# Kernel tuning notes

Measured on AMD Instinct MI355X. Metric: run time of the kernel, lower is better.

The kernel has to match this reference:

```python
import jax, jax.numpy as jnp
import numpy as np

N = 10000       # nodes
F_IN = 512      # input_features
E_DIM = 256     # embedding_features
H0, H1 = 512, 256  # fc layer widths (layers=[512,256]); fc input = 2*E_DIM = 512
N_EDGES = 160000


def setup_inputs() -> dict:
    key = jax.random.key(0)
    ks = jax.random.split(key, 10)
    feature = jax.random.normal(ks[0], (N, F_IN), jnp.float32)
    edge_src = jax.random.randint(ks[1], (N_EDGES,), 0, N, jnp.int32)
    edge_dst = jax.random.randint(ks[2], (N_EDGES,), 0, N, jnp.int32)
    def lin(k, fan_in, fan_out):
        return jax.random.normal(k, (fan_in, fan_out), jnp.float32) / np.sqrt(fan_in).astype(np.float32)
    We = lin(ks[3], F_IN, E_DIM);     be = jnp.zeros((E_DIM,), jnp.float32)
    W0 = lin(ks[4], 2 * E_DIM, H0);   b0 = jnp.zeros((H0,), jnp.float32)
    W1 = lin(ks[5], H0, H1);          b1 = jnp.zeros((H1,), jnp.float32)
    Wlk = lin(ks[6], H1, 1);          blk = jnp.zeros((1,), jnp.float32)
    Wa = lin(ks[7], H1, 2);           ba = jnp.zeros((2,), jnp.float32)
    return dict(feature=feature, We=We, be=be, W0=W0, b0=b0, W1=W1, b1=b1,
                Wlk=Wlk, blk=blk, Wa=Wa, ba=ba,
                edge_src=edge_src, edge_dst=edge_dst)


def reference(feature, We, be, W0, b0, W1, b1, Wlk, blk, Wa, ba, edge_src, edge_dst):
    # get_embedding: Linear + relu
    emb = jax.nn.relu(feature @ We + be)                      # [N, E]
    # Each node i has its neighbor entries plus one 'ending' entry paired with zeros
    seg = jnp.concatenate([edge_src, jnp.arange(N, dtype=edge_src.dtype)])     # [T]
    dst_all = jnp.concatenate([edge_dst, jnp.full((N,), -1, edge_dst.dtype)])  # -1 = ending sentinel
    nbr = jnp.concatenate([emb[edge_dst], jnp.zeros((N, E_DIM), emb.dtype)], axis=0)
    s = jnp.concatenate([emb[seg], nbr], axis=-1)             # [T, 2E]
    # fc MLP, then lk head
    h = jax.nn.relu(jax.nn.relu(s @ W0 + b0) @ W1 + b1)       # [T, H1]
    lk = (h @ Wlk + blk)[:, 0]                                # [T]
    # Deterministic greedy pick per node (argmax of lk == argmax of softmax(lk))
    best = jax.ops.segment_max(lk, seg, num_segments=N)       # [N]
    T = lk.shape[0]
    cand = jnp.where(lk == best[seg], jnp.arange(T, dtype=jnp.int32), -1)
    win = jax.ops.segment_max(cand, seg, num_segments=N)      # winning entry index per node
    chosen = dst_all[win]                                     # chosen neighbor (-1 = ending)
    # action head on the winning pair feature; argmax(softmax(logits)) == argmax(logits)
    logits = h[win] @ Wa + ba                                 # [N, 2]
    at = jnp.argmax(logits, axis=-1)
    do_upd = (chosen >= 0) & (at == 1)
    safe = jnp.clip(chosen, 0, N - 1)
    # hv = mean(feature_origin[i], feature_origin[chosen]) then re-embed
    mean_feat = 0.5 * (feature + feature[safe])               # [N, F]
    new_val = jax.nn.relu(mean_feat @ We + be)                # [N, E]
    tgt = jnp.where(do_upd, safe, N)                          # N = out of range -> dropped
    return emb.at[tgt].set(new_val, mode='drop')
```

## Files before the change

### kernel.cpp

```cpp
#include <hip/hip_runtime.h>
#include <stdint.h>

#define N_NODES 10000
#define F_IN    512
#define E_DIM   256
#define H0D     512
#define H1D     256
#define N_EDGES 160000
#define T_TOT   (N_EDGES + N_NODES)

#define MARGIN_LK 4e-3f
#define MARGIN_L  4e-3f
#define LIST_CAP 60000
#define FIX_GRID 512
#define LP 40

typedef _Float16 f16;
typedef __attribute__((ext_vector_type(8))) _Float16 f16x8;
typedef __attribute__((ext_vector_type(4))) _Float16 f16x4;
typedef __attribute__((ext_vector_type(4))) float f32x4;

__device__ __forceinline__ unsigned int f2ord(float f) {
    unsigned int u = __float_as_uint(f);
    return (u & 0x80000000u) ? ~u : (u | 0x80000000u);
}
__device__ __forceinline__ float ord2f(unsigned int o) {
    unsigned int u = (o & 0x80000000u) ? (o & 0x7fffffffu) : ~o;
    return __uint_as_float(u);
}

__device__ __forceinline__ int seg_of(int t, const int* esrc) {
    return (t < N_EDGES) ? esrc[t] : t - N_EDGES;
}

__global__ void k_prep_all(const float* __restrict__ We,
                           const float* __restrict__ W1,
                           const float* __restrict__ W0,
                           f16* __restrict__ WeC_h, f16* __restrict__ WeC_l,
                           f16* __restrict__ W1C_h, f16* __restrict__ W1C_l,
                           f16* __restrict__ W0C_h, f16* __restrict__ W0C_l) {
    int b = blockIdx.x;
    int n = threadIdx.x;
    const float* W;
    int ld, rowoff, colbase, c;
    f16 *dh_base, *dl_base;
    if (b < 16) {
        W = We; ld = E_DIM; rowoff = 0; colbase = 0; c = b;
        dh_base = WeC_h; dl_base = WeC_l;
    } else if (b < 32) {
        W = W1; ld = H1D; rowoff = 0; colbase = 0; c = b - 16;
        dh_base = W1C_h; dl_base = W1C_l;
    } else {
        int g = (b - 32) >> 3; c = (b - 32) & 7;
        rowoff = (g >= 2) ? 256 : 0; colbase = (g & 1) * 256;
        W = W0; ld = H0D;
        dh_base = W0C_h + (size_t)g * 8 * 256 * 32;
        dl_base = W0C_l + (size_t)g * 8 * 256 * 32;
    }
    f16* dh = dh_base + ((size_t)c * 256 + n) * 32;
    f16* dl = dl_base + ((size_t)c * 256 + n) * 32;
    const float* src = W + (size_t)(rowoff + c * 32) * ld + colbase + n;
#pragma unroll
    for (int kk = 0; kk < 32; kk++) {
        float w = src[(size_t)kk * ld];
        f16 h = (f16)w;
        f16 l = (f16)(w - (float)h);
        dh[kk] = h;
        dl[kk] = l;
    }
}

__global__ __launch_bounds__(256, 2) void k1_split(
        const float* __restrict__ feat, const f16* __restrict__ Bh_g,
        const f16* __restrict__ Bl_g, const float* __restrict__ be,
        float* __restrict__ Z, float* __restrict__ out) {
    __shared__ f16 Ah[32 * LP], Al_[32 * LP];
    const int tid = threadIdx.x;
    const int wave = tid >> 6, lane = tid & 63;
    const int quad = lane >> 4, l15 = lane & 15;
    const int mbase = blockIdx.x * 32;
    const int arow = tid >> 3, apos = tid & 7;
    const int gm_a = mbase + arow;
    const float* Arow = feat + (size_t)gm_a * F_IN + apos * 4;
    const bool rowok = (gm_a < N_NODES);

    f32x4 acc[2][4];
#pragma unroll
    for (int i = 0; i < 2; i++)
#pragma unroll
        for (int j = 0; j < 4; j++) acc[i][j] = (f32x4){0.f, 0.f, 0.f, 0.f};

    f16x8 bh[4], bl[4], bhn[4], bln[4];
#pragma unroll
    for (int ct = 0; ct < 4; ct++) {
        size_t o = ((size_t)(wave * 64 + ct * 16 + l15)) * 32 + quad * 8;
        bh[ct] = *(const f16x8*)(Bh_g + o);
        bl[ct] = *(const f16x8*)(Bl_g + o);
    }
    float4 a = rowok ? *(const float4*)(Arow) : make_float4(0.f, 0.f, 0.f, 0.f);

    for (int c = 0; c < 16; c++) {
        f16x4 hv, lv;
        float av[4] = {a.x, a.y, a.z, a.w};
#pragma unroll
        for (int q = 0; q < 4; q++) {
            f16 h = (f16)av[q];
            hv[q] = h;
            lv[q] = (f16)(av[q] - (float)h);
        }
        *(f16x4*)(Ah + arow * LP + apos * 4) = hv;
        *(f16x4*)(Al_ + arow * LP + apos * 4) = lv;
        if (c + 1 < 16) {
            a = rowok ? *(const float4*)(Arow + (c + 1) * 32)
                      : make_float4(0.f, 0.f, 0.f, 0.f);
#pragma unroll
            for (int ct = 0; ct < 4; ct++) {
                size_t o = ((size_t)((c + 1) * 256 + wave * 64 + ct * 16 + l15)) * 32 + quad * 8;
                bhn[ct] = *(const f16x8*)(Bh_g + o);
                bln[ct] = *(const f16x8*)(Bl_g + o);
            }
        }
        __syncthreads();
        f16x8 afh[2], afl[2];
#pragma unroll
        for (int rt = 0; rt < 2; rt++) {
            afh[rt] = *(const f16x8*)(Ah + (rt * 16 + l15) * LP + quad * 8);
            afl[rt] = *(const f16x8*)(Al_ + (rt * 16 + l15) * LP + quad * 8);
        }
#pragma unroll
        for (int rt = 0; rt < 2; rt++)
#pragma unroll
            for (int ct = 0; ct < 4; ct++) {
                acc[rt][ct] = __builtin_amdgcn_mfma_f32_16x16x32_f16(
                    afh[rt], bh[ct], acc[rt][ct], 0, 0, 0);
                acc[rt][ct] = __builtin_amdgcn_mfma_f32_16x16x32_f16(
                    afl[rt], bh[ct], acc[rt][ct], 0, 0, 0);
                acc[rt][ct] = __builtin_amdgcn_mfma_f32_16x16x32_f16(
                    afh[rt], bl[ct], acc[rt][ct], 0, 0, 0);
            }
        __syncthreads();
#pragma unroll
        for (int ct = 0; ct < 4; ct++) { bh[ct] = bhn[ct]; bl[ct] = bln[ct]; }
    }

#pragma unroll
    for (int ct = 0; ct < 4; ct++) {
        int n = wave * 64 + ct * 16 + l15;
        float bb = be[n];
#pragma unroll
        for (int rt = 0; rt < 2; rt++)
#pragma unroll
            for (int reg = 0; reg < 4; reg++) {
                int gm = mbase + rt * 16 + quad * 4 + reg;
                if (gm < N_NODES) {
                    float z = acc[rt][ct][reg] + bb;
                    Z[(size_t)gm * E_DIM + n] = z;
                    out[(size_t)gm * E_DIM + n] = fmaxf(z, 0.f);
                }
            }
    }
}

__global__ __launch_bounds__(256, 3) void k2_split(
        const float* __restrict__ emb, const f16* __restrict__ W0Ch,
        const f16* __restrict__ W0Cl, const float* __restrict__ b0,
        f16* __restrict__ Ph, f16* __restrict__ Pl,
        f16* __restrict__ Qh, f16* __restrict__ Ql) {
    __shared__ f16 Ah[64 * LP], Al_[64 * LP];
    const int tid = threadIdx.x;
    const int wave = tid >> 6, lane = tid & 63;
    const int quad = lane >> 4, l15 = lane & 15;
    const int mbase = blockIdx.x * 64;
    const int g = blockIdx.y;
    const int isQ = (g >= 2);
    const int colbase = (g & 1) * 256;
    const int arow = tid >> 2, akp = tid & 3;
    const int gm_a = mbase + arow;
    const float* Arow = emb + (size_t)gm_a * E_DIM + akp * 8;
    const bool rowok = (gm_a < N_NODES);
    const f16* Bh_g = W0Ch + (size_t)g * 8 * 256 * 32;
    const f16* Bl_g = W0Cl + (size_t)g * 8 * 256 * 32;

    f32x4 acc[4][4];
#pragma unroll
    for (int i = 0; i < 4; i++)
#pragma unroll
        for (int j = 0; j < 4; j++) acc[i][j] = (f32x4){0.f, 0.f, 0.f, 0.f};

    f16x8 bh[4], bl[4], bhn[4], bln[4];
#pragma unroll
    for (int ct = 0; ct < 4; ct++) {
        size_t o = ((size_t)(wave * 64 + ct * 16 + l15)) * 32 + quad * 8;
        bh[ct] = *(const f16x8*)(Bh_g + o);
        bl[ct] = *(const f16x8*)(Bl_g + o);
    }
    float4 a0 = make_float4(0.f, 0.f, 0.f, 0.f), a1 = a0;
    if (rowok) { a0 = *(const float4*)(Arow); a1 = *(const float4*)(Arow + 4); }

    for (int c = 0; c < 8; c++) {
        f16x8 hv, lv;
        float av[8] = {a0.x, a0.y, a0.z, a0.w, a1.x, a1.y, a1.z, a1.w};
#pragma unroll
        for (int q = 0; q < 8; q++) {
            f16 h = (f16)av[q];
            hv[q] = h;
            lv[q] = (f16)(av[q] - (float)h);
        }
        *(f16x8*)(Ah + arow * LP + akp * 8) = hv;
        *(f16x8*)(Al_ + arow * LP + akp * 8) = lv;
        if (c + 1 < 8) {
            if (rowok) {
                a0 = *(const float4*)(Arow + (c + 1) * 32);
                a1 = *(const float4*)(Arow + (c + 1) * 32 + 4);
            }
#pragma unroll
            for (int ct = 0; ct < 4; ct++) {
                size_t o = ((size_t)((c + 1) * 256 + wave * 64 + ct * 16 + l15)) * 32 + quad * 8;
                bhn[ct] = *(const f16x8*)(Bh_g + o);
                bln[ct] = *(const f16x8*)(Bl_g + o);
            }
        }
        __syncthreads();
        f16x8 afh[4], afl[4];
#pragma unroll
        for (int rt = 0; rt < 4; rt++) {
            afh[rt] = *(const f16x8*)(Ah + (rt * 16 + l15) * LP + quad * 8);
            afl[rt] = *(const f16x8*)(Al_ + (rt * 16 + l15) * LP + quad * 8);
        }
#pragma unroll
        for (int rt = 0; rt < 4; rt++)
#pragma unroll
            for (int ct = 0; ct < 4; ct++) {
                acc[rt][ct] = __builtin_amdgcn_mfma_f32_16x16x32_f16(
                    afh[rt], bh[ct], acc[rt][ct], 0, 0, 0);
                acc[rt][ct] = __builtin_amdgcn_mfma_f32_16x16x32_f16(
                    afl[rt], bh[ct], acc[rt][ct], 0, 0, 0);
                acc[rt][ct] = __builtin_amdgcn_mfma_f32_16x16x32_f16(
                    afh[rt], bl[ct], acc[rt][ct], 0, 0, 0);
            }
        __syncthreads();
#pragma unroll
        for (int ct = 0; ct < 4; ct++) { bh[ct] = bhn[ct]; bl[ct] = bln[ct]; }
    }

    f16* dh = isQ ? Qh : Ph;
    f16* dl = isQ ? Ql : Pl;
#pragma unroll
    for (int ct = 0; ct < 4; ct++) {
        int n = wave * 64 + ct * 16 + l15;
        float bb = isQ ? 0.f : b0[colbase + n];
#pragma unroll
        for (int rt = 0; rt < 4; rt++)
#pragma unroll
            for (int reg = 0; reg < 4; reg++) {
                int gm = mbase + rt * 16 + quad * 4 + reg;
                if (gm < N_NODES) {
                    float v = acc[rt][ct][reg] + bb;
                    f16 h = (f16)v;
                    dh[(size_t)gm * H0D + colbase + n] = h;
                    dl[(size_t)gm * H0D + colbase + n] = (f16)(v - (float)h);
                }
            }
    }
}

__global__ __launch_bounds__(256, 3) void k3_f16(
        const f16* __restrict__ Pf, const f16* __restrict__ Qf,
        const f16* __restrict__ W1Bh, const float* __restrict__ b1,
        const float* __restrict__ Wlk, const float* __restrict__ blkp,
        const float* __restrict__ Wa, const float* __restrict__ ba,
        const int* __restrict__ esrc, const int* __restrict__ edst,
        unsigned long long* __restrict__ keys, float* __restrict__ lk_app,
        float* __restrict__ logits) {
    __shared__ f16 Ah[64 * LP];
    __shared__ float redA[64][5], redB[64][5], redC[64][5];
    __shared__ int s_seg[64], s_dst[64];
    const int tid = threadIdx.x;
    const int wave = tid >> 6, lane = tid & 63;
    const int quad = lane >> 4, l15 = lane & 15;
    const int tbase = blockIdx.x * 64;

    if (tid < 64) {
        int t = tbase + tid;
        int s = 0, d = -1;
        if (t < N_EDGES) { s = esrc[t]; d = edst[t]; }
        else if (t < T_TOT) { s = t - N_EDGES; }
        s_seg[tid] = s;
        s_dst[tid] = d;
    }
    __syncthreads();

    const int arow = tid >> 2, akp = tid & 3;
    const int sA = s_seg[arow], dA = s_dst[arow];
    const f16* Prow = Pf + (size_t)sA * H0D + akp * 8;
    const f16* Qrow = Qf + (size_t)(dA >= 0 ? dA : 0) * H0D + akp * 8;
    const bool hasQ = (dA >= 0);
    const f16x8 zero8 = (f16x8)(f16)0;

    f32x4 acc[4][4];
#pragma unroll
    for (int i = 0; i < 4; i++)
#pragma unroll
        for (int j = 0; j < 4; j++) acc[i][j] = (f32x4){0.f, 0.f, 0.f, 0.f};

    f16x8 pa0 = *(const f16x8*)(Prow);
    f16x8 qa0 = hasQ ? *(const f16x8*)(Qrow) : zero8;
    f16x8 pa1 = *(const f16x8*)(Prow + 32);
    f16x8 qa1 = hasQ ? *(const f16x8*)(Qrow + 32) : zero8;
    f16x8 bf[4], bfn[4];
#pragma unroll
    for (int ct = 0; ct < 4; ct++)
        bf[ct] = *(const f16x8*)(W1Bh + ((size_t)(wave * 64 + ct * 16 + l15)) * 32 + quad * 8);

    for (int c = 0; c < 16; c++) {
        f16x8 hv;
#pragma unroll
        for (int q = 0; q < 8; q++) {
            f16 s = pa0[q] + qa0[q];
            hv[q] = (s > (f16)0) ? s : (f16)0;
        }
        *(f16x8*)(Ah + arow * LP + akp * 8) = hv;
        pa0 = pa1; qa0 = qa1;
        if (c + 2 < 16) {
            pa1 = *(const f16x8*)(Prow + (c + 2) * 32);
            qa1 = hasQ ? *(const f16x8*)(Qrow + (c + 2) * 32) : zero8;
        }
        if (c + 1 < 16) {
#pragma unroll
            for (int ct = 0; ct < 4; ct++)
                bfn[ct] = *(const f16x8*)(W1Bh +
                    ((size_t)((c + 1) * 256 + wave * 64 + ct * 16 + l15)) * 32 + quad * 8);
        }
        __syncthreads();
        f16x8 af[4];
#pragma unroll
        for (int rt = 0; rt < 4; rt++)
            af[rt] = *(const f16x8*)(Ah + (rt * 16 + l15) * LP + quad * 8);
#pragma unroll
        for (int rt = 0; rt < 4; rt++)
#pragma unroll
            for (int ct = 0; ct < 4; ct++)
                acc[rt][ct] = __builtin_amdgcn_mfma_f32_16x16x32_f16(
                    af[rt], bf[ct], acc[rt][ct], 0, 0, 0);
        __syncthreads();
#pragma unroll
        for (int ct = 0; ct < 4; ct++) bf[ct] = bfn[ct];
    }

    float wl[4], wa0[4], wa1[4], bb[4];
#pragma unroll
    for (int ct = 0; ct < 4; ct++) {
        int n = wave * 64 + ct * 16 + l15;
        wl[ct] = Wlk[n];
        wa0[ct] = Wa[2 * n];
        wa1[ct] = Wa[2 * n + 1];
        bb[ct] = b1[n];
    }
#pragma unroll
    for (int rt = 0; rt < 4; rt++) {
#pragma unroll
        for (int reg = 0; reg < 4; reg++) {
            float plk = 0.f, p0 = 0.f, p1 = 0.f;
#pragma unroll
            for (int ct = 0; ct < 4; ct++) {
                float h = fmaxf(acc[rt][ct][reg] + bb[ct], 0.f);
                plk = fmaf(h, wl[ct], plk);
                p0 = fmaf(h, wa0[ct], p0);
                p1 = fmaf(h, wa1[ct], p1);
            }
#pragma unroll
            for (int off = 8; off >= 1; off >>= 1) {
                plk += __shfl_xor(plk, off);
                p0 += __shfl_xor(p0, off);
                p1 += __shfl_xor(p1, off);
            }
            if (l15 == 0) {
                int row = rt * 16 + quad * 4 + reg;
                redA[row][wave] = plk;
                redB[row][wave] = p0;
                redC[row][wave] = p1;
            }
        }
    }
    __syncthreads();
    if (tid < 64) {
        int t = tbase + tid;
        if (t < T_TOT) {
            float lk = redA[tid][0] + redA[tid][1] + redA[tid][2] + redA[tid][3] + blkp[0];
            float l0 = redB[tid][0] + redB[tid][1] + redB[tid][2] + redB[tid][3] + ba[0];
            float l1 = redC[tid][0] + redC[tid][1] + redC[tid][2] + redC[tid][3] + ba[1];
            lk_app[t] = lk;
            logits[2 * t] = l0;
            logits[2 * t + 1] = l1;
            unsigned long long key =
                ((unsigned long long)f2ord(lk) << 32) | (unsigned int)t;
            atomicMax(keys + s_seg[tid], key);
        }
    }
}

__global__ void k_gb(const float* __restrict__ lk_app,
                     const unsigned long long* __restrict__ keys,
                     const int* __restrict__ esrc,
                     const float* __restrict__ logits,
                     int* __restrict__ seg_flag,
                     int* __restrict__ list, int* __restrict__ count) {
    int t = blockIdx.x * 256 + threadIdx.x;
    if (t < T_TOT) {
        int seg = seg_of(t, esrc);
        unsigned long long k = keys[seg];
        int tw = (int)(k & 0xFFFFFFFFull);
        if (t != tw) {
            float best = ord2f((unsigned int)(k >> 32));
            if (lk_app[t] >= best - MARGIN_LK) {
                int idx = atomicAdd(count, 1);
                if (idx < LIST_CAP) list[idx] = t;
                if (atomicExch(seg_flag + seg, 1) == 0) {
                    int idx2 = atomicAdd(count, 1);
                    if (idx2 < LIST_CAP) list[idx2] = tw;
                }
            }
        }
    }
    if (t < N_NODES) {
        int tw = (int)(keys[t] & 0xFFFFFFFFull);
        float g = fabsf(logits[2 * tw + 1] - logits[2 * tw]);
        if (g < MARGIN_L) {
            int idx = atomicAdd(count, 1);
            if (idx < LIST_CAP) list[idx] = tw;
        }
    }
}

__global__ __launch_bounds__(256, 2) void k_fix2(
        const f16* __restrict__ Ph, const f16* __restrict__ Pl,
        const f16* __restrict__ Qh, const f16* __restrict__ Ql,
        const f16* __restrict__ W1Ch, const f16* __restrict__ W1Cl,
        const float* __restrict__ b1, const float* __restrict__ Wlk,
        const float* __restrict__ blkp, const float* __restrict__ Wa,
        const float* __restrict__ ba, const int* __restrict__ esrc,
        const int* __restrict__ edst, const int* __restrict__ list,
        const int* __restrict__ count, unsigned long long* __restrict__ keys2,
        float* __restrict__ logits) {
    __shared__ f16 Ah[64 * LP], Al_[64 * LP];
    __shared__ float redA[64][5], redB[64][5], redC[64][5];
    __shared__ int s_seg[64], s_dst[64], s_t[64];
    const int tid = threadIdx.x;
    const int wave = tid >> 6, lane = tid & 63;
    const int quad = lane >> 4, l15 = lane & 15;
    int cnt = *count;
    if (cnt > LIST_CAP) cnt = LIST_CAP;
    const int nch = (cnt + 63) / 64;

    for (int ch = blockIdx.x; ch < nch; ch += gridDim.x) {
        if (tid < 64) {
            int li = ch * 64 + tid;
            int t = (li < cnt) ? list[li] : -1;
            int s = 0, d = -1;
            if (t >= 0 && t < T_TOT) {
                if (t < N_EDGES) { s = esrc[t]; d = edst[t]; }
                else { s = t - N_EDGES; }
            } else t = -1;
            s_t[tid] = t;
            s_seg[tid] = s;
            s_dst[tid] = d;
        }
        __syncthreads();

        const int arow = tid >> 2, akp = tid & 3;
        const int sA = s_seg[arow], dA = s_dst[arow];
        const f16* ph = Ph + (size_t)sA * H0D + akp * 8;
        const f16* pl = Pl + (size_t)sA * H0D + akp * 8;
        const f16* qh = Qh + (size_t)(dA >= 0 ? dA : 0) * H0D + akp * 8;
        const f16* ql = Ql + (size_t)(dA >= 0 ? dA : 0) * H0D + akp * 8;
        const bool hasQ = (dA >= 0);

        f32x4 acc[4][4];
#pragma unroll
        for (int i = 0; i < 4; i++)
#pragma unroll
            for (int j = 0; j < 4; j++) acc[i][j] = (f32x4){0.f, 0.f, 0.f, 0.f};

        for (int c = 0; c < 16; c++) {
            f16x8 vh = *(const f16x8*)(ph + c * 32);
            f16x8 vl = *(const f16x8*)(pl + c * 32);
            f16x8 wh, wlq;
            if (hasQ) {
                wh = *(const f16x8*)(qh + c * 32);
                wlq = *(const f16x8*)(ql + c * 32);
            }
            f16x8 hv, lv;
#pragma unroll
            for (int q = 0; q < 8; q++) {
                float v = (float)vh[q] + (float)vl[q];
                if (hasQ) v += (float)wh[q] + (float)wlq[q];
                v = fmaxf(v, 0.f);
                f16 h = (f16)v;
                hv[q] = h;
                lv[q] = (f16)(v - (float)h);
            }
            *(f16x8*)(Ah + arow * LP + akp * 8) = hv;
            *(f16x8*)(Al_ + arow * LP + akp * 8) = lv;
            f16x8 bh[4], bl[4];
#pragma unroll
            for (int ct = 0; ct < 4; ct++) {
                size_t o = ((size_t)(c * 256 + wave * 64 + ct * 16 + l15)) * 32 + quad * 8;
                bh[ct] = *(const f16x8*)(W1Ch + o);
                bl[ct] = *(const f16x8*)(W1Cl + o);
            }
            __syncthreads();
            f16x8 afh[4], afl[4];
#pragma unroll
            for (int rt = 0; rt < 4; rt++) {
                afh[rt] = *(const f16x8*)(Ah + (rt * 16 + l15) * LP + quad * 8);
                afl[rt] = *(const f16x8*)(Al_ + (rt * 16 + l15) * LP + quad * 8);
            }
#pragma unroll
            for (int rt = 0; rt < 4; rt++)
#pragma unroll
                for (int ct = 0; ct < 4; ct++) {
                    acc[rt][ct] = __builtin_amdgcn_mfma_f32_16x16x32_f16(
                        afh[rt], bh[ct], acc[rt][ct], 0, 0, 0);
                    acc[rt][ct] = __builtin_amdgcn_mfma_f32_16x16x32_f16(
                        afl[rt], bh[ct], acc[rt][ct], 0, 0, 0);
                    acc[rt][ct] = __builtin_amdgcn_mfma_f32_16x16x32_f16(
                        afh[rt], bl[ct], acc[rt][ct], 0, 0, 0);
                }
            __syncthreads();
        }

        float wl[4], wa0[4], wa1[4], bb[4];
#pragma unroll
        for (int ct = 0; ct < 4; ct++) {
            int n = wave * 64 + ct * 16 + l15;
            wl[ct] = Wlk[n];
            wa0[ct] = Wa[2 * n];
            wa1[ct] = Wa[2 * n + 1];
            bb[ct] = b1[n];
        }
#pragma unroll
        for (int rt = 0; rt < 4; rt++) {
#pragma unroll
            for (int reg = 0; reg < 4; reg++) {
                float plk = 0.f, p0 = 0.f, p1 = 0.f;
#pragma unroll
                for (int ct = 0; ct < 4; ct++) {
                    float h = fmaxf(acc[rt][ct][reg] + bb[ct], 0.f);
                    plk = fmaf(h, wl[ct], plk);
                    p0 = fmaf(h, wa0[ct], p0);
                    p1 = fmaf(h, wa1[ct], p1);
                }
#pragma unroll
                for (int off = 8; off >= 1; off >>= 1) {
                    plk += __shfl_xor(plk, off);
                    p0 += __shfl_xor(p0, off);
                    p1 += __shfl_xor(p1, off);
                }
                if (l15 == 0) {
                    int row = rt * 16 + quad * 4 + reg;
                    redA[row][wave] = plk;
                    redB[row][wave] = p0;
                    redC[row][wave] = p1;
                }
            }
        }
        __syncthreads();
        if (tid < 64) {
            int t = s_t[tid];
            if (t >= 0) {
                float lk = redA[tid][0] + redA[tid][1] + redA[tid][2] + redA[tid][3] + blkp[0];
                float l0 = redB[tid][0] + redB[tid][1] + redB[tid][2] + redB[tid][3] + ba[0];
                float l1 = redC[tid][0] + redC[tid][1] + redC[tid][2] + redC[tid][3] + ba[1];
                logits[2 * t] = l0;
                logits[2 * t + 1] = l1;
                unsigned long long key =
                    ((unsigned long long)f2ord(lk) << 32) | (unsigned int)t;
                atomicMax(keys2 + s_seg[tid], key);
            }
        }
        __syncthreads();
    }
}

__global__ void k4_select(const unsigned long long* __restrict__ keys,
                          const unsigned long long* __restrict__ keys2,
                          const int* __restrict__ edst,
                          const float* __restrict__ logits,
                          int* __restrict__ chosen_arr,
                          int* __restrict__ tgt_writer) {
    int i = blockIdx.x * 256 + threadIdx.x;
    if (i >= N_NODES) return;
    unsigned long long key = keys[i];
    unsigned long long k2v = keys2[i];
    if (k2v != 0ull) key = k2v;
    int t = (int)(key & 0xFFFFFFFFull);
    int chosen = (t < N_EDGES) ? edst[t] : -1;
    float lg0 = logits[2 * t], lg1 = logits[2 * t + 1];
    int at1 = (lg1 > lg0) ? 1 : 0;
    int c = (chosen >= 0 && at1) ? chosen : -1;
    chosen_arr[i] = c;
    if (c >= 0) atomicMax(tgt_writer + c, i + 1);
}

__global__ void k5_update(const int* __restrict__ chosen_arr,
                          const int* __restrict__ tgt_writer,
                          const float* __restrict__ Z,
                          float* __restrict__ out) {
    int i = blockIdx.x;
    int c = chosen_arr[i];
    if (c < 0 || tgt_writer[c] != i + 1) return;
    int n = threadIdx.x;
    float z = 0.5f * (Z[(size_t)i * E_DIM + n] + Z[(size_t)c * E_DIM + n]);
    out[(size_t)c * E_DIM + n] = fmaxf(z, 0.f);
}

extern "C" void kernel_launch(void* const* d_in, const int* in_sizes, int n_in,
                              void* d_out, int out_size, void* d_ws,
                              size_t ws_size, hipStream_t stream) {
    const float* feat = (const float*)d_in[0];
    const float* We   = (const float*)d_in[1];
    const float* be   = (const float*)d_in[2];
    const float* W0   = (const float*)d_in[3];
    const float* b0   = (const float*)d_in[4];
    const float* W1   = (const float*)d_in[5];
    const float* b1   = (const float*)d_in[6];
    const float* Wlk  = (const float*)d_in[7];
    const float* blkp = (const float*)d_in[8];
    const float* Wa   = (const float*)d_in[9];
    const float* ba   = (const float*)d_in[10];
    const int* esrc   = (const int*)d_in[11];
    const int* edst   = (const int*)d_in[12];
    float* out = (float*)d_out;

    char* ws = (char*)d_ws;
    size_t off = 0;
    float* Z  = (float*)(ws + off); off += (size_t)N_NODES * E_DIM * 4;
    f16* Ph   = (f16*)(ws + off);   off += (size_t)N_NODES * H0D * 2;
    f16* Pl   = (f16*)(ws + off);   off += (size_t)N_NODES * H0D * 2;
    f16* Qh   = (f16*)(ws + off);   off += (size_t)N_NODES * H0D * 2;
    f16* Ql   = (f16*)(ws + off);   off += (size_t)N_NODES * H0D * 2;
    char* zero_base = ws + off;
    unsigned long long* keys  = (unsigned long long*)(ws + off); off += N_NODES * 8;
    unsigned long long* keys2 = (unsigned long long*)(ws + off); off += N_NODES * 8;
    int* tgt_writer = (int*)(ws + off); off += N_NODES * 4;
    int* seg_flag   = (int*)(ws + off); off += N_NODES * 4;
    int* count      = (int*)(ws + off); off += 128;
    size_t zero_bytes = (size_t)((ws + off) - zero_base);
    float* logits = (float*)(ws + off); off += (size_t)T_TOT * 2 * 4;
    float* lk_app = (float*)(ws + off); off += (size_t)T_TOT * 4;
    int* list     = (int*)(ws + off); off += (size_t)LIST_CAP * 4;
    int* chosen_arr = (int*)(ws + off); off += N_NODES * 4;
    f16* WeC_h = (f16*)(ws + off); off += (size_t)16 * 256 * 32 * 2;
    f16* WeC_l = (f16*)(ws + off); off += (size_t)16 * 256 * 32 * 2;
    f16* W1C_h = (f16*)(ws + off); off += (size_t)16 * 256 * 32 * 2;
    f16* W1C_l = (f16*)(ws + off); off += (size_t)16 * 256 * 32 * 2;
    f16* W0C_h = (f16*)(ws + off); off += (size_t)32 * 256 * 32 * 2;
    f16* W0C_l = (f16*)(ws + off); off += (size_t)32 * 256 * 32 * 2;

    hipMemsetAsync(zero_base, 0, zero_bytes, stream);

    k_prep_all<<<dim3(64), 256, 0, stream>>>(
        We, W1, W0, WeC_h, WeC_l, W1C_h, W1C_l, W0C_h, W0C_l);
    k1_split<<<dim3((N_NODES + 31) / 32), 256, 0, stream>>>(
        feat, WeC_h, WeC_l, be, Z, out);
    k2_split<<<dim3((N_NODES + 63) / 64, 4), 256, 0, stream>>>(
        out, W0C_h, W0C_l, b0, Ph, Pl, Qh, Ql);
    k3_f16<<<dim3((T_TOT + 63) / 64), 256, 0, stream>>>(
        Ph, Qh, W1C_h, b1, Wlk, blkp, Wa, ba, esrc, edst,
        keys, lk_app, logits);
    k_gb<<<dim3((T_TOT + 255) / 256), 256, 0, stream>>>(
        lk_app, keys, esrc, logits, seg_flag, list, count);
    k_fix2<<<dim3(FIX_GRID), 256, 0, stream>>>(
        Ph, Pl, Qh, Ql, W1C_h, W1C_l, b1, Wlk, blkp, Wa, ba,
        esrc, edst, list, count, keys2, logits);
    k4_select<<<dim3((N_NODES + 255) / 256), 256, 0, stream>>>(
        keys, keys2, edst, logits, chosen_arr, tgt_writer);
    k5_update<<<dim3(N_NODES), 256, 0, stream>>>(chosen_arr, tgt_writer, Z, out);
}
```

Before: 279.4 us.

## Load A fragments directly from global in k3, drop LDS staging and barriers

Each wave now gathers its own P/Q rows straight into MFMA A fragments and applies add+relu in registers. This removes the shared-memory tile and both per-chunk __syncthreads, along with the software prefetch double-buffering of the P/Q and W1 loads. In exchange each of the 4 waves redundantly loads the same 64 rows, so global/L2 gather traffic for A rises about fourfold. Load latency is no longer hidden by explicit prefetching.

```diff
diff --git a/kernel.cpp b/kernel.cpp
--- a/kernel.cpp
+++ b/kernel.cpp
@@ -272,7 +272,6 @@
         const int* __restrict__ esrc, const int* __restrict__ edst,
         unsigned long long* __restrict__ keys, float* __restrict__ lk_app,
         float* __restrict__ logits) {
-    __shared__ f16 Ah[64 * LP];
     __shared__ float redA[64][5], redB[64][5], redC[64][5];
     __shared__ int s_seg[64], s_dst[64];
     const int tid = threadIdx.x;
@@ -290,11 +289,17 @@
     }
     __syncthreads();
 
-    const int arow = tid >> 2, akp = tid & 3;
-    const int sA = s_seg[arow], dA = s_dst[arow];
-    const f16* Prow = Pf + (size_t)sA * H0D + akp * 8;
-    const f16* Qrow = Qf + (size_t)(dA >= 0 ? dA : 0) * H0D + akp * 8;
-    const bool hasQ = (dA >= 0);
+    const f16* prow[4];
+    const f16* qrow[4];
+    bool hq[4];
+#pragma unroll
+    for (int rt = 0; rt < 4; rt++) {
+        int r = rt * 16 + l15;
+        int s = s_seg[r], d = s_dst[r];
+        prow[rt] = Pf + (size_t)s * H0D + quad * 8;
+        hq[rt] = (d >= 0);
+        qrow[rt] = Qf + (size_t)(d >= 0 ? d : 0) * H0D + quad * 8;
+    }
     const f16x8 zero8 = (f16x8)(f16)0;
 
     f32x4 acc[4][4];
@@ -303,48 +308,28 @@
 #pragma unroll
         for (int j = 0; j < 4; j++) acc[i][j] = (f32x4){0.f, 0.f, 0.f, 0.f};
 
-    f16x8 pa0 = *(const f16x8*)(Prow);
-    f16x8 qa0 = hasQ ? *(const f16x8*)(Qrow) : zero8;
-    f16x8 pa1 = *(const f16x8*)(Prow + 32);
-    f16x8 qa1 = hasQ ? *(const f16x8*)(Qrow + 32) : zero8;
-    f16x8 bf[4], bfn[4];
-#pragma unroll
-    for (int ct = 0; ct < 4; ct++)
-        bf[ct] = *(const f16x8*)(W1Bh + ((size_t)(wave * 64 + ct * 16 + l15)) * 32 + quad * 8);
-
     for (int c = 0; c < 16; c++) {
-        f16x8 hv;
-#pragma unroll
-        for (int q = 0; q < 8; q++) {
-            f16 s = pa0[q] + qa0[q];
-            hv[q] = (s > (f16)0) ? s : (f16)0;
-        }
-        *(f16x8*)(Ah + arow * LP + akp * 8) = hv;
-        pa0 = pa1; qa0 = qa1;
-        if (c + 2 < 16) {
-            pa1 = *(const f16x8*)(Prow + (c + 2) * 32);
-            qa1 = hasQ ? *(const f16x8*)(Qrow + (c + 2) * 32) : zero8;
-        }
-        if (c + 1 < 16) {
-#pragma unroll
-            for (int ct = 0; ct < 4; ct++)
-                bfn[ct] = *(const f16x8*)(W1Bh +
-                    ((size_t)((c + 1) * 256 + wave * 64 + ct * 16 + l15)) * 32 + quad * 8);
-        }
-        __syncthreads();
-        f16x8 af[4];
-#pragma unroll
-        for (int rt = 0; rt < 4; rt++)
-            af[rt] = *(const f16x8*)(Ah + (rt * 16 + l15) * LP + quad * 8);
+        f16x8 af[4], bf[4];
+#pragma unroll
+        for (int rt = 0; rt < 4; rt++) {
+            f16x8 pa = *(const f16x8*)(prow[rt] + c * 32);
+            f16x8 qa = hq[rt] ? *(const f16x8*)(qrow[rt] + c * 32) : zero8;
+#pragma unroll
+            for (int q = 0; q < 8; q++) {
+                f16 s = pa[q] + qa[q];
+                af[rt][q] = (s > (f16)0) ? s : (f16)0;
+            }
+        }
+#pragma unroll
+        for (int ct = 0; ct < 4; ct++)
+            bf[ct] = *(const f16x8*)(W1Bh +
+                ((size_t)(c * 256 + wave * 64 + ct * 16 + l15)) * 32 + quad * 8);
 #pragma unroll
         for (int rt = 0; rt < 4; rt++)
 #pragma unroll
             for (int ct = 0; ct < 4; ct++)
                 acc[rt][ct] = __builtin_amdgcn_mfma_f32_16x16x32_f16(
                     af[rt], bf[ct], acc[rt][ct], 0, 0, 0);
-        __syncthreads();
-#pragma unroll
-        for (int ct = 0; ct < 4; ct++) bf[ct] = bfn[ct];
     }
 
     float wl[4], wa0[4], wa1[4], bb[4];
```

After: 400.4 us. +43.3%, slower.
